# Kernel tuning notes

Measured on AMD Instinct MI355X. Metric: run time of the kernel, lower is better.

## Reference

```python
import jax, jax.numpy as jnp
import numpy as np

B, S, D, H = 2, 2048, 1024, 16
HS = D // H  # head size 64
EPS = 1e-5


def setup_inputs() -> dict:
    key = jax.random.key(0)
    ks = jax.random.split(key, 12)
    s = lambda fan_in: 1.0 / np.sqrt(fan_in)
    return {
        "x": jax.random.normal(ks[0], (B, S, D), dtype=jnp.float32),
        # per-head QKV weights, math orientation [H, D, HS] (x @ W)
        "wq": jax.random.normal(ks[1], (H, D, HS), dtype=jnp.float32) * s(D),
        "wk": jax.random.normal(ks[2], (H, D, HS), dtype=jnp.float32) * s(D),
        "wv": jax.random.normal(ks[3], (H, D, HS), dtype=jnp.float32) * s(D),
        "wproj": jax.random.normal(ks[4], (D, D), dtype=jnp.float32) * s(D),
        "bproj": jnp.zeros((D,), dtype=jnp.float32),
        "w1": jax.random.normal(ks[5], (D, 4 * D), dtype=jnp.float32) * s(D),
        "b1": jnp.zeros((4 * D,), dtype=jnp.float32),
        "w2": jax.random.normal(ks[6], (4 * D, D), dtype=jnp.float32) * s(4 * D),
        "b2": jnp.zeros((D,), dtype=jnp.float32),
        "ln1_g": jnp.ones((D,), dtype=jnp.float32),
        "ln1_b": jnp.zeros((D,), dtype=jnp.float32),
        "ln2_g": jnp.ones((D,), dtype=jnp.float32),
        "ln2_b": jnp.zeros((D,), dtype=jnp.float32),
    }


def _layernorm(x, g, b):
    mu = jnp.mean(x, axis=-1, keepdims=True)
    var = jnp.mean(jnp.square(x - mu), axis=-1, keepdims=True)
    return (x - mu) * jax.lax.rsqrt(var + EPS) * g + b


def reference(x, wq, wk, wv, wproj, bproj, w1, b1, w2, b2, ln1_g, ln1_b, ln2_g, ln2_b):
    Bq, T, C = x.shape
    xn = _layernorm(x, ln1_g, ln1_b)
    # per-head projections, batched over heads
    q = jnp.einsum('btd,hdk->bhtk', xn, wq)
    k = jnp.einsum('btd,hdk->bhtk', xn, wk)
    v = jnp.einsum('btd,hdk->bhtk', xn, wv)
    scale = k.shape[-1] ** (-0.5)
    scores = jnp.einsum('bhtk,bhsk->bhts', q, k) * scale  # [B,H,T,T]
    causal = jnp.tril(jnp.ones((T, T), dtype=bool))
    scores = jnp.where(causal, scores, -jnp.inf)
    att = jax.nn.softmax(scores, axis=-1)
    out = jnp.einsum('bhts,bhsk->bhtk', att, v)  # [B,H,T,HS]
    out = out.transpose(0, 2, 1, 3).reshape(Bq, T, C)  # concat heads
    attn_out = out @ wproj + bproj
    h = x + attn_out
    hn = _layernorm(h, ln2_g, ln2_b)
    ff = jax.nn.relu(hn @ w1 + b1) @ w2 + b2
    return h + ff
```

## Files before the change

### kernel.cpp

```cpp
#include <hip/hip_runtime.h>


typedef __bf16 bf16_t;
typedef __attribute__((ext_vector_type(8))) __bf16 bf16x8;
typedef __attribute__((ext_vector_type(4))) __bf16 bf16x4;
typedef __attribute__((ext_vector_type(4))) float f32x4;

__device__ __forceinline__ f32x4 mfma16(bf16x8 a, bf16x8 b, f32x4 c) {
  return __builtin_amdgcn_mfma_f32_16x16x32_bf16(a, b, c, 0, 0, 0);
}

__device__ __forceinline__ void gll16(const void* g, void* l) {
  __builtin_amdgcn_global_load_lds(
      (const __attribute__((address_space(1))) void*)g,
      (__attribute__((address_space(3))) void*)l, 16, 0, 0);
}

__global__ __launch_bounds__(256) void ln_kernel(
    const float* __restrict__ x, const float* __restrict__ g,
    const float* __restrict__ be, bf16_t* __restrict__ out) {
  const int row = blockIdx.x;
  const int tid = threadIdx.x;
  const float4 v = *(reinterpret_cast<const float4*>(x + (size_t)row * 1024) + tid);
  float s1 = v.x + v.y + v.z + v.w;
  float s2 = v.x * v.x + v.y * v.y + v.z * v.z + v.w * v.w;
#pragma unroll
  for (int off = 1; off < 64; off <<= 1) {
    s1 += __shfl_xor(s1, off);
    s2 += __shfl_xor(s2, off);
  }
  __shared__ float red[8];
  const int l = tid & 63, w = tid >> 6;
  if (l == 0) { red[w] = s1; red[w + 4] = s2; }
  __syncthreads();
  s1 = red[0] + red[1] + red[2] + red[3];
  s2 = red[4] + red[5] + red[6] + red[7];
  const float mu = s1 * (1.f / 1024.f);
  const float var = s2 * (1.f / 1024.f) - mu * mu;
  const float rstd = rsqrtf(var + 1e-5f);
  const float4 gg = *(reinterpret_cast<const float4*>(g) + tid);
  const float4 bb = *(reinterpret_cast<const float4*>(be) + tid);
  bf16x4 o;
  o[0] = (bf16_t)((v.x - mu) * rstd * gg.x + bb.x);
  o[1] = (bf16_t)((v.y - mu) * rstd * gg.y + bb.y);
  o[2] = (bf16_t)((v.z - mu) * rstd * gg.z + bb.z);
  o[3] = (bf16_t)((v.w - mu) * rstd * gg.w + bb.w);
  *(reinterpret_cast<bf16x4*>(out + (size_t)row * 1024) + tid) = o;
}

__global__ __launch_bounds__(256) void ln2_red_kernel(
    const float* __restrict__ p, const float* __restrict__ bp,
    const float* __restrict__ x, const float* __restrict__ g,
    const float* __restrict__ be, float* __restrict__ hb,
    bf16_t* __restrict__ out) {
  const size_t PM = (size_t)4096 * 1024;
  const int row = blockIdx.x;
  const int tid = threadIdx.x;
  const size_t ro = (size_t)row * 1024;
  float4 v = *(reinterpret_cast<const float4*>(p + ro) + tid);
  const float4 v1 = *(reinterpret_cast<const float4*>(p + PM + ro) + tid);
  const float4 vb = *(reinterpret_cast<const float4*>(bp) + tid);
  const float4 vx = *(reinterpret_cast<const float4*>(x + ro) + tid);
  v.x += v1.x + vb.x + vx.x; v.y += v1.y + vb.y + vx.y;
  v.z += v1.z + vb.z + vx.z; v.w += v1.w + vb.w + vx.w;
  *(reinterpret_cast<float4*>(hb + ro) + tid) = v;
  float s1 = v.x + v.y + v.z + v.w;
  float s2 = v.x * v.x + v.y * v.y + v.z * v.z + v.w * v.w;
#pragma unroll
  for (int off = 1; off < 64; off <<= 1) {
    s1 += __shfl_xor(s1, off);
    s2 += __shfl_xor(s2, off);
  }
  __shared__ float red[8];
  const int l = tid & 63, w = tid >> 6;
  if (l == 0) { red[w] = s1; red[w + 4] = s2; }
  __syncthreads();
  s1 = red[0] + red[1] + red[2] + red[3];
  s2 = red[4] + red[5] + red[6] + red[7];
  const float mu = s1 * (1.f / 1024.f);
  const float var = s2 * (1.f / 1024.f) - mu * mu;
  const float rstd = rsqrtf(var + 1e-5f);
  const float4 gg = *(reinterpret_cast<const float4*>(g) + tid);
  const float4 bb = *(reinterpret_cast<const float4*>(be) + tid);
  bf16x4 o;
  o[0] = (bf16_t)((v.x - mu) * rstd * gg.x + bb.x);
  o[1] = (bf16_t)((v.y - mu) * rstd * gg.y + bb.y);
  o[2] = (bf16_t)((v.z - mu) * rstd * gg.z + bb.z);
  o[3] = (bf16_t)((v.w - mu) * rstd * gg.w + bb.w);
  *(reinterpret_cast<bf16x4*>(out + ro) + tid) = o;
}

__global__ __launch_bounds__(256) void red4_kernel(
    const float* __restrict__ p, const float* __restrict__ b2,
    const float* __restrict__ hb, float* __restrict__ out) {
  const size_t PM = (size_t)4096 * 1024;
  const int row = blockIdx.x;
  const int tid = threadIdx.x;
  const size_t ro = (size_t)row * 1024;
  float4 v = *(reinterpret_cast<const float4*>(p + ro) + tid);
#pragma unroll
  for (int s = 1; s < 4; s++) {
    const float4 vs = *(reinterpret_cast<const float4*>(p + s * PM + ro) + tid);
    v.x += vs.x; v.y += vs.y; v.z += vs.z; v.w += vs.w;
  }
  const float4 vb = *(reinterpret_cast<const float4*>(b2) + tid);
  const float4 vh = *(reinterpret_cast<const float4*>(hb + ro) + tid);
  v.x += vb.x + vh.x; v.y += vb.y + vh.y;
  v.z += vb.z + vh.z; v.w += vb.w + vh.w;
  *(reinterpret_cast<float4*>(out + ro) + tid) = v;
}

__global__ __launch_bounds__(256) void transpose_cvt(
    const float* __restrict__ in, bf16_t* __restrict__ out, int R, int C) {
  __shared__ float t[32][33];
  const int bz = blockIdx.z;
  in += (size_t)bz * R * C;
  out += (size_t)bz * R * C;
  const int c0 = blockIdx.x * 32, r0 = blockIdx.y * 32;
  const int tx = threadIdx.x, ty = threadIdx.y;
#pragma unroll
  for (int i = 0; i < 4; i++)
    t[ty + i * 8][tx] = in[(size_t)(r0 + ty + i * 8) * C + c0 + tx];
  __syncthreads();
#pragma unroll
  for (int i = 0; i < 4; i++)
    out[(size_t)(c0 + ty + i * 8) * R + r0 + tx] = (bf16_t)t[tx][ty + i * 8];
}

template <int MODE>
__global__ __launch_bounds__(256) void gemm_bt(
    const bf16_t* __restrict__ A, const bf16_t* __restrict__ BT,
    const float* __restrict__ bias, const float* __restrict__ resid,
    void* __restrict__ out0, void* __restrict__ out1, int M, int N, int K) {
  __shared__ __align__(16) bf16_t Al[128 * 32];
  __shared__ __align__(16) bf16_t Bl[128 * 32];
  const int tid = threadIdx.x;
  const int l = tid & 63, w = tid >> 6;
  const int wr = w >> 1, wc = w & 1;
  const int lr = l & 15, lg = l >> 4;
  const int gx = gridDim.x;
  const int nwg = gx * gridDim.y;
  int flat = blockIdx.y * gx + blockIdx.x;
  flat = (flat & 7) * (nwg >> 3) + (flat >> 3);
  const int bm = (flat / gx) * 128, bn = (flat % gx) * 128;

  int k0 = 0, nK = K >> 5;
  if constexpr (MODE == 3) {
    const int chunk = K / gridDim.z;
    k0 = blockIdx.z * chunk;
    nK = chunk >> 5;
  }

  f32x4 acc[4][4];
#pragma unroll
  for (int i = 0; i < 4; i++)
#pragma unroll
    for (int j = 0; j < 4; j++) acc[i][j] = (f32x4)(0.f);

  const char* Ag = (const char*)(A + (size_t)bm * K + k0);
  const char* Bg = (const char*)(BT + (size_t)bn * K + k0);
  const size_t rowb = (size_t)K * 2;

  for (int kt = 0; kt < nK; ++kt) {
#pragma unroll
    for (int i = 0; i < 2; i++) {
      const int s = i * 256 + tid;
      const size_t go = (size_t)(s >> 2) * rowb + (size_t)(kt * 64 + (s & 3) * 16);
      gll16(Ag + go, (char*)Al + (i * 256 + w * 64) * 16);
      gll16(Bg + go, (char*)Bl + (i * 256 + w * 64) * 16);
    }
    __syncthreads();
    bf16x8 af[4], bfr[4];
#pragma unroll
    for (int mi = 0; mi < 4; mi++)
      af[mi] = *reinterpret_cast<const bf16x8*>(Al + (wr * 64 + mi * 16 + lr) * 32 + lg * 8);
#pragma unroll
    for (int ni = 0; ni < 4; ni++)
      bfr[ni] = *reinterpret_cast<const bf16x8*>(Bl + (wc * 64 + ni * 16 + lr) * 32 + lg * 8);
#pragma unroll
    for (int mi = 0; mi < 4; mi++)
#pragma unroll
      for (int ni = 0; ni < 4; ni++)
        acc[mi][ni] = mfma16(af[mi], bfr[ni], acc[mi][ni]);
    __syncthreads();
  }

#pragma unroll
  for (int mi = 0; mi < 4; mi++) {
    const int r = bm + wr * 64 + mi * 16 + lg * 4;
#pragma unroll
    for (int ni = 0; ni < 4; ni++) {
      const int c = bn + wc * 64 + ni * 16 + lr;
      f32x4 v = acc[mi][ni];
      if constexpr (MODE == 1) {
        const float bb = bias[c];
        float* o = (float*)out0;
#pragma unroll
        for (int j = 0; j < 4; j++)
          o[(size_t)(r + j) * N + c] = v[j] + bb + resid[(size_t)(r + j) * N + c];
      } else if constexpr (MODE == 2) {
        const float bb = bias[c];
        bf16_t* o = (bf16_t*)out0;
#pragma unroll
        for (int j = 0; j < 4; j++)
          o[(size_t)(r + j) * N + c] = (bf16_t)fmaxf(v[j] + bb, 0.f);
      } else if constexpr (MODE == 3) {
        float* o = (float*)out0 + (size_t)blockIdx.z * M * N;
#pragma unroll
        for (int j = 0; j < 4; j++)
          o[(size_t)(r + j) * N + c] = v[j];
      } else {
        if (c < 2048) {
          bf16_t* o = (bf16_t*)out0;
#pragma unroll
          for (int j = 0; j < 4; j++)
            o[(size_t)(r + j) * 2048 + c] = (bf16_t)v[j];
        } else {
          const int nn = c - 2048;
          const int bI = r >> 11, tl = r & 2047;
          bf16x4 pk;
#pragma unroll
          for (int j = 0; j < 4; j++) pk[j] = (bf16_t)v[j];
          *reinterpret_cast<bf16x4*>((bf16_t*)out1 +
              ((size_t)(bI * 1024 + nn)) * 2048 + tl) = pk;
        }
      }
    }
  }
}

__device__ __forceinline__ void attn_tile(
    const bf16_t* __restrict__ kl, const bf16_t* __restrict__ vl,
    bf16_t* __restrict__ plw, const bf16x8* qf, f32x4* oacc,
    float* mrow, float* lrow, const int lr, const int lg,
    const int rbase, const int cbase, const bool diag) {
  f32x4 sc4[4];
#pragma unroll
  for (int ct = 0; ct < 4; ct++) sc4[ct] = (f32x4)(0.f);
#pragma unroll
  for (int ct = 0; ct < 4; ct++)
#pragma unroll
    for (int kc = 0; kc < 2; kc++) {
      bf16x8 kf = *reinterpret_cast<const bf16x8*>(
          &kl[(ct * 16 + lr) * 72 + kc * 32 + lg * 8]);
      sc4[ct] = mfma16(qf[kc], kf, sc4[ct]);
    }
#pragma unroll
  for (int ct = 0; ct < 4; ct++)
#pragma unroll
    for (int j = 0; j < 4; j++) {
      float sv = sc4[ct][j] * 0.125f;
      if (diag && (cbase + ct * 16 + lr > rbase + j)) sv = -1e30f;
      sc4[ct][j] = sv;
    }
  float rmax[4];
#pragma unroll
  for (int j = 0; j < 4; j++)
    rmax[j] = fmaxf(fmaxf(sc4[0][j], sc4[1][j]), fmaxf(sc4[2][j], sc4[3][j]));
#pragma unroll
  for (int off = 1; off < 16; off <<= 1)
#pragma unroll
    for (int j = 0; j < 4; j++) rmax[j] = fmaxf(rmax[j], __shfl_xor(rmax[j], off));
  float fac[4];
#pragma unroll
  for (int j = 0; j < 4; j++) {
    const float mn = fmaxf(mrow[j], rmax[j]);
    fac[j] = __expf(mrow[j] - mn);
    mrow[j] = mn;
  }
  float rsum[4] = {0.f, 0.f, 0.f, 0.f};
#pragma unroll
  for (int ct = 0; ct < 4; ct++)
#pragma unroll
    for (int j = 0; j < 4; j++) {
      const float pv = __expf(sc4[ct][j] - mrow[j]);
      sc4[ct][j] = pv;
      rsum[j] += pv;
    }
#pragma unroll
  for (int off = 1; off < 16; off <<= 1)
#pragma unroll
    for (int j = 0; j < 4; j++) rsum[j] += __shfl_xor(rsum[j], off);
#pragma unroll
  for (int j = 0; j < 4; j++) lrow[j] = lrow[j] * fac[j] + rsum[j];
#pragma unroll
  for (int ht = 0; ht < 4; ht++)
#pragma unroll
    for (int j = 0; j < 4; j++) oacc[ht][j] *= fac[j];
#pragma unroll
  for (int ct = 0; ct < 4; ct++)
#pragma unroll
    for (int j = 0; j < 4; j++)
      plw[(lg * 4 + j) * 72 + ct * 16 + lr] = (bf16_t)sc4[ct][j];
  bf16x8 pf[2];
#pragma unroll
  for (int sc = 0; sc < 2; sc++)
    pf[sc] = *reinterpret_cast<const bf16x8*>(&plw[lr * 72 + sc * 32 + lg * 8]);
#pragma unroll
  for (int ht = 0; ht < 4; ht++)
#pragma unroll
    for (int sc = 0; sc < 2; sc++) {
      bf16x8 vf = *reinterpret_cast<const bf16x8*>(
          &vl[(ht * 16 + lr) * 72 + sc * 32 + lg * 8]);
      oacc[ht] = mfma16(pf[sc], vf, oacc[ht]);
    }
}

template <int SPLIT>
__global__ __launch_bounds__(256) void attn_kernel(
    const bf16_t* __restrict__ qk, const bf16_t* __restrict__ vT,
    bf16_t* __restrict__ ac, float* __restrict__ po,
    float* __restrict__ mlb) {
  const int f = blockIdx.x;
  const int bh = (f & 7) + 8 * ((f >> 3) & 3);
  const int p = (f >> 5) & 15;
  const int half = SPLIT ? (f >> 9) : 0;
  const int qlo = p, qhi = 31 - p;
  const int nst = qhi + 1;
  const int kcut = SPLIT ? (p >= 7 ? 8 : 16 - p) : nst;
  const int st0 = half ? kcut : 0;
  const int st1 = half ? nst : kcut;
  const int b = bh >> 4, h = bh & 15;
  const int tid = threadIdx.x;
  const int l = tid & 63, w = tid >> 6;
  const int lr = l & 15, lg = l >> 4;

  __shared__ __align__(16) bf16_t kl[64 * 72];
  __shared__ __align__(16) bf16_t vl[64 * 72];
  __shared__ __align__(16) bf16_t pl[4][16 * 72];
  bf16_t* plw = pl[w];

  const bf16_t* qb = qk + ((size_t)(b * 2048 + w * 16 + lr)) * 2048 + h * 64;
  bf16x8 qfl[2], qfh[2];
#pragma unroll
  for (int kc = 0; kc < 2; kc++) {
    qfl[kc] = *(const bf16x8*)(qb + (size_t)qlo * 64 * 2048 + kc * 32 + lg * 8);
    qfh[kc] = *(const bf16x8*)(qb + (size_t)qhi * 64 * 2048 + kc * 32 + lg * 8);
  }

  f32x4 oaccl[4], oacch[4];
  float ml[4], llo[4], mh[4], lhi[4];
#pragma unroll
  for (int i = 0; i < 4; i++) { oaccl[i] = (f32x4)(0.f); oacch[i] = (f32x4)(0.f); }
#pragma unroll
  for (int j = 0; j < 4; j++) { ml[j] = -1e30f; llo[j] = 0.f; mh[j] = -1e30f; lhi[j] = 0.f; }

  const int rlo = qlo * 64 + w * 16 + lg * 4;
  const int rhi = qhi * 64 + w * 16 + lg * 4;

  const int r0 = tid >> 3, c0 = (tid & 7) * 8;
  const bf16_t* kg = qk + ((size_t)(b * 2048)) * 2048 + 1024 + h * 64;
  const bf16_t* vg = vT + ((size_t)(bh * 64)) * 2048;

  bf16x8 kreg[2], vreg[2];
#pragma unroll
  for (int i = 0; i < 2; i++) {
    const int r = r0 + i * 32;
    kreg[i] = *(const bf16x8*)(kg + (size_t)(st0 * 64 + r) * 2048 + c0);
    vreg[i] = *(const bf16x8*)(vg + (size_t)r * 2048 + st0 * 64 + c0);
  }

  for (int st = st0; st < st1; ++st) {
    __syncthreads();
#pragma unroll
    for (int i = 0; i < 2; i++) {
      const int r = r0 + i * 32;
      *(bf16x8*)(&kl[r * 72 + c0]) = kreg[i];
      *(bf16x8*)(&vl[r * 72 + c0]) = vreg[i];
    }
    __syncthreads();
    if (st + 1 < st1) {
#pragma unroll
      for (int i = 0; i < 2; i++) {
        const int r = r0 + i * 32;
        kreg[i] = *(const bf16x8*)(kg + (size_t)((st + 1) * 64 + r) * 2048 + c0);
        vreg[i] = *(const bf16x8*)(vg + (size_t)r * 2048 + (st + 1) * 64 + c0);
      }
    }
    attn_tile(kl, vl, plw, qfh, oacch, mh, lhi, lr, lg, rhi, st * 64, st == qhi);
    if (st <= qlo)
      attn_tile(kl, vl, plw, qfl, oaccl, ml, llo, lr, lg, rlo, st * 64, st == qlo);
  }

  if constexpr (SPLIT == 0) {
#pragma unroll
    for (int ht = 0; ht < 4; ht++)
#pragma unroll
      for (int j = 0; j < 4; j++) {
        const size_t tl = (size_t)(b * 2048 + rlo + j);
        ac[tl * 1024 + h * 64 + ht * 16 + lr] = (bf16_t)(oaccl[ht][j] / llo[j]);
        const size_t th = (size_t)(b * 2048 + rhi + j);
        ac[th * 1024 + h * 64 + ht * 16 + lr] = (bf16_t)(oacch[ht][j] / lhi[j]);
      }
  } else {
    float* poh = po + (size_t)half * 65536 * 64;
    const size_t base = (size_t)bh * 2048;
#pragma unroll
    for (int ht = 0; ht < 4; ht++)
#pragma unroll
      for (int j = 0; j < 4; j++) {
        poh[(base + rlo + j) * 64 + ht * 16 + lr] = oaccl[ht][j];
        poh[(base + rhi + j) * 64 + ht * 16 + lr] = oacch[ht][j];
      }
    if (lr == 0) {
      float2* mlh = (float2*)mlb + (size_t)half * 65536 + base;
#pragma unroll
      for (int j = 0; j < 4; j++) {
        mlh[rlo + j] = make_float2(ml[j], llo[j]);
        mlh[rhi + j] = make_float2(mh[j], lhi[j]);
      }
    }
  }
}

__global__ __launch_bounds__(256) void attn_combine(
    const float* __restrict__ po, const float* __restrict__ mlb,
    bf16_t* __restrict__ ac) {
  const int t = threadIdx.x;
  const int row = blockIdx.x * 16 + (t >> 4);
  const int hs4 = (t & 15) * 4;
  const size_t HALF = (size_t)65536 * 64;
  const float2 ml0 = ((const float2*)mlb)[row];
  const float2 ml1 = ((const float2*)mlb)[65536 + row];
  const float m = fmaxf(ml0.x, ml1.x);
  const float w0 = __expf(ml0.x - m), w1 = __expf(ml1.x - m);
  const float inv = 1.f / (ml0.y * w0 + ml1.y * w1);
  const float4 o0 = *(const float4*)(po + (size_t)row * 64 + hs4);
  const float4 o1 = *(const float4*)(po + HALF + (size_t)row * 64 + hs4);
  const int bh = row >> 11, qr = row & 2047;
  const int b = bh >> 4, h = bh & 15;
  bf16x4 o;
  o[0] = (bf16_t)((o0.x * w0 + o1.x * w1) * inv);
  o[1] = (bf16_t)((o0.y * w0 + o1.y * w1) * inv);
  o[2] = (bf16_t)((o0.z * w0 + o1.z * w1) * inv);
  o[3] = (bf16_t)((o0.w * w0 + o1.w * w1) * inv);
  *(bf16x4*)(ac + ((size_t)(b * 2048 + qr)) * 1024 + h * 64 + hs4) = o;
}

extern "C" void kernel_launch(void* const* d_in, const int* in_sizes, int n_in,
                              void* d_out, int out_size, void* d_ws, size_t ws_size,
                              hipStream_t stream) {
  const float* x     = (const float*)d_in[0];
  const float* wq    = (const float*)d_in[1];
  const float* wk    = (const float*)d_in[2];
  const float* wv    = (const float*)d_in[3];
  const float* wproj = (const float*)d_in[4];
  const float* bproj = (const float*)d_in[5];
  const float* w1    = (const float*)d_in[6];
  const float* b1    = (const float*)d_in[7];
  const float* w2    = (const float*)d_in[8];
  const float* b2    = (const float*)d_in[9];
  const float* ln1g  = (const float*)d_in[10];
  const float* ln1b  = (const float*)d_in[11];
  const float* ln2g  = (const float*)d_in[12];
  const float* ln2b  = (const float*)d_in[13];
  float* out = (float*)d_out;

  char* ws = (char*)d_ws;
  const size_t MB = 1 << 20;
  bf16_t* xn  = (bf16_t*)(ws + 0);
  bf16_t* wT  = (bf16_t*)(ws + 8 * MB);
  float*  hbuf= (float*)(ws + 16 * MB);
  bf16_t* qkb = (bf16_t*)(ws + 32 * MB);
  bf16_t* vTb = (bf16_t*)(ws + 48 * MB);
  bf16_t* acb = (bf16_t*)(ws + 56 * MB);
  bf16_t* ffa = (bf16_t*)(ws + 32 * MB);
  float*  part= (float*)(ws + 64 * MB);
  float*  po  = (float*)(ws + 64 * MB);
  float*  mlb = (float*)(ws + 96 * MB);
  bf16_t* hn  = xn;

  const bool big = ws_size >= 128 * MB;
  dim3 tb(32, 8);

  ln_kernel<<<4096, 256, 0, stream>>>(x, ln1g, ln1b, xn);
  transpose_cvt<<<dim3(2, 32, 16), tb, 0, stream>>>(wq, wT, 1024, 64);
  transpose_cvt<<<dim3(2, 32, 16), tb, 0, stream>>>(wk, wT + 1024 * 1024, 1024, 64);
  transpose_cvt<<<dim3(2, 32, 16), tb, 0, stream>>>(wv, wT + 2048 * 1024, 1024, 64);
  gemm_bt<0><<<dim3(24, 32), 256, 0, stream>>>(xn, wT, nullptr, nullptr, qkb, vTb,
                                               4096, 3072, 1024);
  if (big) {
    attn_kernel<1><<<1024, 256, 0, stream>>>(qkb, vTb, acb, po, mlb);
    attn_combine<<<4096, 256, 0, stream>>>(po, mlb, acb);
  } else {
    attn_kernel<0><<<512, 256, 0, stream>>>(qkb, vTb, acb, nullptr, nullptr);
  }
  transpose_cvt<<<dim3(32, 32, 1), tb, 0, stream>>>(wproj, wT, 1024, 1024);
  if (big) {
    gemm_bt<3><<<dim3(8, 32, 2), 256, 0, stream>>>(acb, wT, nullptr, nullptr,
                                                   part, nullptr, 4096, 1024, 1024);
    ln2_red_kernel<<<4096, 256, 0, stream>>>(part, bproj, x, ln2g, ln2b, hbuf, hn);
  } else {
    gemm_bt<1><<<dim3(8, 32), 256, 0, stream>>>(acb, wT, bproj, x, hbuf, nullptr,
                                                4096, 1024, 1024);
    ln_kernel<<<4096, 256, 0, stream>>>(hbuf, ln2g, ln2b, hn);
  }
  transpose_cvt<<<dim3(128, 32, 1), tb, 0, stream>>>(w1, wT, 1024, 4096);
  gemm_bt<2><<<dim3(32, 32), 256, 0, stream>>>(hn, wT, b1, nullptr, ffa, nullptr,
                                               4096, 4096, 1024);
  transpose_cvt<<<dim3(32, 128, 1), tb, 0, stream>>>(w2, wT, 4096, 1024);
  if (big) {
    gemm_bt<3><<<dim3(8, 32, 4), 256, 0, stream>>>(ffa, wT, nullptr, nullptr,
                                                   part, nullptr, 4096, 1024, 4096);
    red4_kernel<<<4096, 256, 0, stream>>>(part, b2, hbuf, out);
  } else {
    gemm_bt<1><<<dim3(8, 32), 256, 0, stream>>>(ffa, wT, b2, hbuf, out, nullptr,
                                                4096, 1024, 4096);
  }
}
```

Before: 424.7 us.

## Read K and V fragments directly from global memory in attention

Removes the shared-memory staging of K and V tiles, along with the register prefetch and the two barriers per key tile, in the attention kernel. Each wave now loads its MFMA operand fragments for K and V straight from global memory, relying on L1/L2 to serve the loads that all four waves share. This drops the LDS traffic and block-wide synchronisation, but each K/V fragment is now fetched by every wave rather than once per block. It also loses the software prefetch that overlapped the next tile's loads with compute.

```diff
diff --git a/kernel.cpp b/kernel.cpp
--- a/kernel.cpp
+++ b/kernel.cpp
@@ -230,10 +230,11 @@
 }
 
 __device__ __forceinline__ void attn_tile(
-    const bf16_t* __restrict__ kl, const bf16_t* __restrict__ vl,
-    bf16_t* __restrict__ plw, const bf16x8* qf, f32x4* oacc,
+    const bf16_t* __restrict__ kg2, const bf16_t* __restrict__ vg,
+    const int st, bf16_t* __restrict__ plw, const bf16x8* qf, f32x4* oacc,
     float* mrow, float* lrow, const int lr, const int lg,
-    const int rbase, const int cbase, const bool diag) {
+    const int rbase, const bool diag) {
+  const int cbase = st * 64;
   f32x4 sc4[4];
 #pragma unroll
   for (int ct = 0; ct < 4; ct++) sc4[ct] = (f32x4)(0.f);
@@ -241,8 +242,8 @@
   for (int ct = 0; ct < 4; ct++)
 #pragma unroll
     for (int kc = 0; kc < 2; kc++) {
-      bf16x8 kf = *reinterpret_cast<const bf16x8*>(
-          &kl[(ct * 16 + lr) * 72 + kc * 32 + lg * 8]);
+      const bf16x8 kf = *reinterpret_cast<const bf16x8*>(
+          kg2 + (size_t)(cbase + ct * 16 + lr) * 2048 + kc * 32 + lg * 8);
       sc4[ct] = mfma16(qf[kc], kf, sc4[ct]);
     }
 #pragma unroll
@@ -300,8 +301,8 @@
   for (int ht = 0; ht < 4; ht++)
 #pragma unroll
     for (int sc = 0; sc < 2; sc++) {
-      bf16x8 vf = *reinterpret_cast<const bf16x8*>(
-          &vl[(ht * 16 + lr) * 72 + sc * 32 + lg * 8]);
+      const bf16x8 vf = *reinterpret_cast<const bf16x8*>(
+          vg + (size_t)(ht * 16 + lr) * 2048 + cbase + sc * 32 + lg * 8);
       oacc[ht] = mfma16(pf[sc], vf, oacc[ht]);
     }
 }
@@ -325,8 +326,6 @@
   const int l = tid & 63, w = tid >> 6;
   const int lr = l & 15, lg = l >> 4;
 
-  __shared__ __align__(16) bf16_t kl[64 * 72];
-  __shared__ __align__(16) bf16_t vl[64 * 72];
   __shared__ __align__(16) bf16_t pl[4][16 * 72];
   bf16_t* plw = pl[w];
 
@@ -348,38 +347,13 @@
   const int rlo = qlo * 64 + w * 16 + lg * 4;
   const int rhi = qhi * 64 + w * 16 + lg * 4;
 
-  const int r0 = tid >> 3, c0 = (tid & 7) * 8;
-  const bf16_t* kg = qk + ((size_t)(b * 2048)) * 2048 + 1024 + h * 64;
+  const bf16_t* kg2 = qk + ((size_t)(b * 2048)) * 2048 + 1024 + h * 64;
   const bf16_t* vg = vT + ((size_t)(bh * 64)) * 2048;
 
-  bf16x8 kreg[2], vreg[2];
-#pragma unroll
-  for (int i = 0; i < 2; i++) {
-    const int r = r0 + i * 32;
-    kreg[i] = *(const bf16x8*)(kg + (size_t)(st0 * 64 + r) * 2048 + c0);
-    vreg[i] = *(const bf16x8*)(vg + (size_t)r * 2048 + st0 * 64 + c0);
-  }
-
   for (int st = st0; st < st1; ++st) {
-    __syncthreads();
-#pragma unroll
-    for (int i = 0; i < 2; i++) {
-      const int r = r0 + i * 32;
-      *(bf16x8*)(&kl[r * 72 + c0]) = kreg[i];
-      *(bf16x8*)(&vl[r * 72 + c0]) = vreg[i];
-    }
-    __syncthreads();
-    if (st + 1 < st1) {
-#pragma unroll
-      for (int i = 0; i < 2; i++) {
-        const int r = r0 + i * 32;
-        kreg[i] = *(const bf16x8*)(kg + (size_t)((st + 1) * 64 + r) * 2048 + c0);
-        vreg[i] = *(const bf16x8*)(vg + (size_t)r * 2048 + (st + 1) * 64 + c0);
-      }
-    }
-    attn_tile(kl, vl, plw, qfh, oacch, mh, lhi, lr, lg, rhi, st * 64, st == qhi);
+    attn_tile(kg2, vg, st, plw, qfh, oacch, mh, lhi, lr, lg, rhi, st == qhi);
     if (st <= qlo)
-      attn_tile(kl, vl, plw, qfl, oaccl, ml, llo, lr, lg, rlo, st * 64, st == qlo);
+      attn_tile(kg2, vg, st, plw, qfl, oaccl, ml, llo, lr, lg, rlo, st == qlo);
   }
 
   if constexpr (SPLIT == 0) {
```

Result: slower. 449.8 us (+5.9%).
